# Optimization experiments

Hardware: AMD Instinct MI355X
Metric: run time of the kernel (lower is better)

Reference implementation:

```python
import jax, jax.numpy as jnp
import numpy as np

B = 16; C = 20; M = 64
LEVELS = [("p3", 8, 128), ("p4", 16, 64), ("p5", 32, 32)]  # name, stride, H(=W)
BOUNDS = {"p3": (0.0, 64.0), "p4": (64.0, 128.0), "p5": (128.0, jnp.inf)}
TOPK = 1000; MAX_DET = 100; IOU_THR = 0.5; SCORE_THR = 0.3


def _grid(h, w, stride):
    # replicates get_fpn_location_coords (incl. torch's meshgrid(y, x) ordering)
    xs = stride * (jnp.arange(w, dtype=jnp.float32) + 0.5)
    ys = stride * (jnp.arange(h, dtype=jnp.float32) + 0.5)
    a, b = jnp.meshgrid(ys, xs, indexing="ij")
    return jnp.stack([a, b], axis=-1).reshape(h * w, 2)


def setup_inputs() -> dict:
    key = jax.random.key(0)
    ks = jax.random.split(key, 16)
    inp = {}
    inp["locs_p3"] = _grid(128, 128, 8)
    inp["locs_p4"] = _grid(64, 64, 16)
    inp["locs_p5"] = _grid(32, 32, 32)
    xy = jax.random.uniform(ks[0], (B, M, 2), minval=0.0, maxval=700.0)
    wh = jax.random.uniform(ks[1], (B, M, 2), minval=32.0, maxval=300.0)
    cid = jax.random.randint(ks[2], (B, M, 1), 0, C).astype(jnp.float32)
    gt = jnp.concatenate([xy, xy + wh, cid], axis=-1)
    pad = jnp.arange(M) >= (M - 16)  # last 16 rows are background padding
    inp["gt_boxes"] = jnp.where(pad[None, :, None], -1.0, gt)
    for i, (name, stride, h) in enumerate(LEVELS):
        n = h * h
        inp[f"cls_{name}"] = jax.random.normal(ks[3 + i], (B, n, C)) - 2.0
        inp[f"reg_{name}"] = jax.random.uniform(ks[6 + i], (B, n, 4), minval=0.0, maxval=8.0)
        inp[f"ctr_{name}"] = jax.random.normal(ks[9 + i], (B, n))
    return inp


def _match_level(centers, gt, lower, upper):
    # centers (N,2), gt (M,5) -> matched gt box per center (N,5), -1 for background
    x = centers[:, 0:1]; y = centers[:, 1:2]
    x0, y0, x1, y1 = gt[:, 0], gt[:, 1], gt[:, 2], gt[:, 3]
    ltrb = jnp.stack([x - x0[None], y - y0[None], x1[None] - x, y1[None] - y], axis=-1)  # (N,M,4)
    inside = ltrb.min(-1) > 0
    maxd = ltrb.max(-1)
    ok = inside & (maxd > lower) & (maxd < upper)
    areas = (x1 - x0) * (y1 - y0)
    quality = ok.astype(jnp.float32) * (1e8 - areas)[None, :]
    q = quality.max(-1)
    idx = jnp.argmax(quality, axis=-1)
    idx = jnp.where(q < 1e-5, -1, idx)
    matched = gt[jnp.clip(idx, 0)]
    return jnp.where((idx < 0)[:, None], -1.0, matched)


def _targets(centers, matched, stride):
    # fcos_get_deltas_from_locations + fcos_make_centerness_targets
    xc, yc = centers[:, 0], centers[:, 1]
    d = jnp.stack([(xc - matched[:, 0]) / stride, (yc - matched[:, 1]) / stride,
                   (matched[:, 2] - xc) / stride, (matched[:, 3] - yc) / stride], axis=1)
    bg = jnp.all(matched == -1.0, axis=1)
    d = jnp.where(bg[:, None], -1.0, d)
    l, t, r, b = d[:, 0], d[:, 1], d[:, 2], d[:, 3]
    ctr = jnp.sqrt(jnp.minimum(l, r) * jnp.minimum(t, b) / (jnp.maximum(l, r) * jnp.maximum(t, b)))
    ctr = jnp.where(jnp.all(d == -1.0, axis=1), -1.0, ctr)
    return d, ctr


def _decode(deltas, locs, stride):
    # fcos_apply_deltas_to_locations
    d = jnp.maximum(deltas, 0.0)
    xc, yc = locs[:, 0], locs[:, 1]
    return jnp.stack([xc - d[:, 0] * stride, yc - d[:, 1] * stride,
                      xc + d[:, 2] * stride, yc + d[:, 3] * stride], axis=1)


def _nms_keep(boxes, scores, valid):
    # sequential greedy NMS (argmax + IoU suppression), capped at MAX_DET picks
    areas = (boxes[:, 2] - boxes[:, 0]) * (boxes[:, 3] - boxes[:, 1])
    def body(_, state):
        active, keep = state
        s = jnp.where(active, scores, -jnp.inf)
        i = jnp.argmax(s)
        ok = s[i] > -jnp.inf
        b = boxes[i]
        xx1 = jnp.maximum(b[0], boxes[:, 0]); yy1 = jnp.maximum(b[1], boxes[:, 1])
        xx2 = jnp.minimum(b[2], boxes[:, 2]); yy2 = jnp.minimum(b[3], boxes[:, 3])
        inter = jnp.clip(xx2 - xx1, 0.0) * jnp.clip(yy2 - yy1, 0.0)
        iou = inter / (areas[i] + areas - inter)
        keep = keep.at[i].set(keep[i] | ok)
        active = jnp.where(ok, active & (iou <= IOU_THR), active)
        return active, keep
    _, keep = jax.lax.fori_loop(0, MAX_DET, body, (valid, jnp.zeros_like(valid)))
    return keep


def _infer_one(boxes, scores_cls):
    # boxes (N,4), scores_cls (N,C) -> masked detections (TOPK,5)
    score = scores_cls.max(-1)
    cls_id = jnp.argmax(scores_cls, axis=-1)
    sc, idx = jax.lax.top_k(score, TOPK)
    bx = boxes[idx]; cid = cls_id[idx]
    valid = sc > SCORE_THR
    max_coord = jnp.max(jnp.where(valid[:, None], bx, 0.0))
    off = cid.astype(bx.dtype) * (max_coord + 1.0)  # class_spec_nms offsets
    keep = _nms_keep(bx + off[:, None], sc, valid)
    det = jnp.concatenate([bx, sc[:, None]], axis=-1)
    return jnp.where(keep[:, None], det, 0.0)


def reference(locs_p3, locs_p4, locs_p5, gt_boxes, cls_p3, cls_p4, cls_p5,
              reg_p3, reg_p4, reg_p5, ctr_p3, ctr_p4, ctr_p5):
    locs = {"p3": locs_p3, "p4": locs_p4, "p5": locs_p5}
    cls = {"p3": cls_p3, "p4": cls_p4, "p5": cls_p5}
    reg = {"p3": reg_p3, "p4": reg_p4, "p5": reg_p5}
    ctr = {"p3": ctr_p3, "p4": ctr_p4, "p5": ctr_p5}
    # ---- training targets (no-grad in original) ----
    tgt_d, tgt_c = [], []
    for name, stride, _ in LEVELS:
        lo, hi = BOUNDS[name]
        matched = jax.vmap(lambda g, L=locs[name], lo=lo, hi=hi: _match_level(L, g, lo, hi))(gt_boxes)
        d, c = jax.vmap(lambda m, L=locs[name], s=stride: _targets(L, m, s))(matched)
        tgt_d.append(d); tgt_c.append(c)
    gt_deltas = jax.lax.stop_gradient(jnp.concatenate(tgt_d, axis=1))   # (B, N_total, 4)
    gt_ctr = jax.lax.stop_gradient(jnp.concatenate(tgt_c, axis=1))      # (B, N_total)
    # ---- inference: decode + score + class-specific NMS ----
    all_boxes, all_scores = [], []
    for name, stride, _ in LEVELS:
        bx = jax.vmap(lambda d, L=locs[name], s=stride: _decode(d, L, s))(reg[name])
        sc = jnp.sqrt(jax.nn.sigmoid(cls[name]) * jax.nn.sigmoid(ctr[name])[..., None])
        all_boxes.append(bx); all_scores.append(sc)
    boxes = jnp.concatenate(all_boxes, axis=1)    # (B, N_total, 4)
    scores = jnp.concatenate(all_scores, axis=1)  # (B, N_total, C)
    dets = jax.vmap(_infer_one)(boxes, scores)    # (B, TOPK, 5)
    return dets, gt_deltas, gt_ctr
```

## Files before the change

kernel.cpp:

```cpp
#include <hip/hip_runtime.h>
#include <hip/hip_bf16.h>
#include <math.h>
#include <stdint.h>

#pragma clang fp contract(off)

#define NB   16
#define NC   20
#define NM   64
#define NT   21504
#define OFF1 16384
#define OFF2 20480
#define TOPK 1000
#define DELTA_OFF 80000L
#define CTR_OFF   1456256L

#define WS_SCORES   0L
#define WS_BOXESW   344064L
#define WS_CIDW     1720320L
#define WS_TOPSC    2064384L
#define WS_TOPBOX   2080768L
#define WS_TOPSHIFT 2146304L
#define WS_TOPAREA  2211840L
#define WS_ACT      2228224L
#define WS_MATRIX   0L

__device__ __forceinline__ int detect_bf(const void* locs0) {
  unsigned w = *(const unsigned*)locs0;
  return ((w & 0xFFFFu) == 0u) ? 0 : 1;
}
__device__ __forceinline__ float ldin(const void* p, long i, int bf) {
  if (bf) return __uint_as_float(((unsigned)((const unsigned short*)p)[i]) << 16);
  return ((const float*)p)[i];
}
__device__ __forceinline__ unsigned short f2bf(float v) {
  unsigned w = __float_as_uint(v);
  return (unsigned short)((w + 0x7FFFu + ((w >> 16) & 1u)) >> 16);
}
__device__ __forceinline__ void stout(void* p, long i, float v, int bf) {
  if (bf) ((unsigned short*)p)[i] = f2bf(v);
  else    ((float*)p)[i] = v;
}

__global__ __launch_bounds__(256)
void k_main(const void* locs0, const void* locs1, const void* locs2,
            const void* gt,
            const void* cls0, const void* cls1, const void* cls2,
            const void* reg0, const void* reg1, const void* reg2,
            const void* ctr0, const void* ctr1, const void* ctr2,
            void* out, float* scores, float* boxesw, float* cidw) {
  __shared__ float sgt[NM * 5];
  __shared__ float scls[256 * 21];
  const int bf  = detect_bf(locs0);
  const int b   = blockIdx.y;
  const int blk = blockIdx.x;
  const int tid = threadIdx.x;
  const int n   = blk * 256 + tid;

  const void *L, *CL, *RG, *CT; int NL, base; float stride, lower, upper;
  if (blk < 64)      { L=locs0; CL=cls0; RG=reg0; CT=ctr0; NL=16384; base=0;    stride=8.f;  lower=0.f;   upper=64.f; }
  else if (blk < 80) { L=locs1; CL=cls1; RG=reg1; CT=ctr1; NL=4096;  base=OFF1; stride=16.f; lower=64.f;  upper=128.f; }
  else               { L=locs2; CL=cls2; RG=reg2; CT=ctr2; NL=1024;  base=OFF2; stride=32.f; lower=128.f; upper=INFINITY; }
  const int nl     = n - base;
  const int nlBase = blk * 256 - base;

  for (int i = tid; i < NM * 5; i += 256) sgt[i] = ldin(gt, (long)b * NM * 5 + i, bf);

  long cbase = ((long)b * NL + nlBase) * NC;
  if (!bf) {
    const float4* p = (const float4*)((const float*)CL + cbase);
    for (int i = tid; i < 1280; i += 256) {
      float4 v = p[i];
      int e = i * 4;
      scls[( e      / 20) * 21 +  e      % 20] = v.x;
      scls[((e + 1) / 20) * 21 + (e + 1) % 20] = v.y;
      scls[((e + 2) / 20) * 21 + (e + 2) % 20] = v.z;
      scls[((e + 3) / 20) * 21 + (e + 3) % 20] = v.w;
    }
  } else {
    const unsigned* p = (const unsigned*)((const unsigned short*)CL + cbase);
    for (int i = tid; i < 2560; i += 256) {
      unsigned w = p[i];
      int e = i * 2;
      scls[( e      / 20) * 21 +  e      % 20] = __uint_as_float((w & 0xFFFFu) << 16);
      scls[((e + 1) / 20) * 21 + (e + 1) % 20] = __uint_as_float(w & 0xFFFF0000u);
    }
  }
  __syncthreads();

  float cx = ldin(L, (long)nl * 2 + 0, bf);
  float cy = ldin(L, (long)nl * 2 + 1, bf);

  float best = -1.0f; int bi = 0;
  for (int m = 0; m < NM; ++m) {
    float g0 = sgt[m*5+0], g1 = sgt[m*5+1], g2 = sgt[m*5+2], g3 = sgt[m*5+3];
    float l = cx - g0, t = cy - g1, r = g2 - cx, d = g3 - cy;
    float mn = fminf(fminf(l, t), fminf(r, d));
    float mx = fmaxf(fmaxf(l, t), fmaxf(r, d));
    bool  ok = (mn > 0.f) && (mx > lower) && (mx < upper);
    float area = (g2 - g0) * (g3 - g1);
    float q = ok ? (100000000.0f - area) : 0.f;
    if (q > best) { best = q; bi = m; }
  }
  float d0, d1, d2, d3, ctrv;
  if (best < 1e-5f) {
    d0 = d1 = d2 = d3 = -1.f; ctrv = -1.f;
  } else {
    float m0 = sgt[bi*5+0], m1 = sgt[bi*5+1], m2 = sgt[bi*5+2], m3 = sgt[bi*5+3];
    d0 = (cx - m0) / stride; d1 = (cy - m1) / stride;
    d2 = (m2 - cx) / stride; d3 = (m3 - cy) / stride;
    float mnlr = fminf(d0, d2), mntb = fminf(d1, d3);
    float mxlr = fmaxf(d0, d2), mxtb = fmaxf(d1, d3);
    ctrv = sqrtf((mnlr * mntb) / (mxlr * mxtb));
  }
  long dbase = DELTA_OFF + ((long)b * NT + n) * 4;
  if (!bf) {
    *(float4*)((float*)out + dbase) = make_float4(d0, d1, d2, d3);
  } else {
    ushort4 v; v.x = f2bf(d0); v.y = f2bf(d1); v.z = f2bf(d2); v.w = f2bf(d3);
    *(ushort4*)((unsigned short*)out + dbase) = v;
  }
  stout(out, CTR_OFF + (long)b * NT + n, ctrv, bf);

  float ct  = ldin(CT, (long)b * NL + nl, bf);
  float sct = 1.0f / (1.0f + expf(-ct));
  float smax = -1.0f; int ci = 0;
  for (int c = 0; c < NC; ++c) {
    float v  = scls[tid * 21 + c];
    float sv = 1.0f / (1.0f + expf(-v));
    float s  = sqrtf(sv * sct);
    if (s > smax) { smax = s; ci = c; }
  }
  float r0, r1, r2, r3;
  long rbase = ((long)b * NL + nl) * 4;
  if (!bf) {
    float4 rv = *(const float4*)((const float*)RG + rbase);
    r0 = rv.x; r1 = rv.y; r2 = rv.z; r3 = rv.w;
  } else {
    uint2 rw = *(const uint2*)((const unsigned short*)RG + rbase);
    r0 = __uint_as_float((rw.x & 0xFFFFu) << 16); r1 = __uint_as_float(rw.x & 0xFFFF0000u);
    r2 = __uint_as_float((rw.y & 0xFFFFu) << 16); r3 = __uint_as_float(rw.y & 0xFFFF0000u);
  }
  r0 = fmaxf(r0, 0.f); r1 = fmaxf(r1, 0.f); r2 = fmaxf(r2, 0.f); r3 = fmaxf(r3, 0.f);
  long o = (long)b * NT + n;
  scores[o] = smax;
  *(float4*)(boxesw + o * 4) =
      make_float4(cx - r0 * stride, cy - r1 * stride, cx + r2 * stride, cy + r3 * stride);
  cidw[o] = (float)ci;
}

__global__ __launch_bounds__(1024)
void k_select(const float* scores, const float* boxesw, const float* cidw,
              float* topScore, float* topBox, float* topShift, float* topArea,
              unsigned long long* actInit) {
  const int b    = blockIdx.x;
  const int tid  = threadIdx.x;
  const int wid  = tid >> 6;
  const int lane = tid & 63;
  const float* sb = scores + (long)b * NT;

  __shared__ unsigned long long selKeys[1024];
  __shared__ unsigned wcnt[16][3];
  __shared__ unsigned selCnt;
  __shared__ float redf[16];
  __shared__ float sMaxC;

  unsigned inv[21];
#pragma unroll
  for (int k = 0; k < 21; ++k)
    inv[k] = ~__float_as_uint(sb[tid + k * 1024]);

  unsigned V = 0xC0000000u;
  for (int s = 28; s >= 0; s -= 2) {
    unsigned T1 = V | (1u << s), T2 = V | (2u << s), T3 = V | (3u << s);
    unsigned c1 = 0, c2 = 0, c3 = 0;
#pragma unroll
    for (int k = 0; k < 21; ++k) {
      c1 += (unsigned)__popcll(__ballot(inv[k] < T1));
      c2 += (unsigned)__popcll(__ballot(inv[k] < T2));
      c3 += (unsigned)__popcll(__ballot(inv[k] < T3));
    }
    if (lane == 0) { wcnt[wid][0] = c1; wcnt[wid][1] = c2; wcnt[wid][2] = c3; }
    __syncthreads();
    unsigned t1 = 0, t2 = 0, t3 = 0;
    for (int w = 0; w < 16; ++w) { t1 += wcnt[w][0]; t2 += wcnt[w][1]; t3 += wcnt[w][2]; }
    unsigned p = (t3 < TOPK) ? 3u : (t2 < TOPK) ? 2u : (t1 < TOPK) ? 1u : 0u;
    V |= p << s;
    __syncthreads();
  }

  if (tid == 0) selCnt = 0u;
  __syncthreads();
#pragma unroll
  for (int k = 0; k < 21; ++k)
    if (inv[k] < V) {
      unsigned p = atomicAdd(&selCnt, 1u);
      if (p < 1024u) selKeys[p] = ((unsigned long long)inv[k] << 32) | (unsigned)(tid + k * 1024);
    }
  __syncthreads();
#pragma unroll
  for (int k = 0; k < 21; ++k)
    if (inv[k] == V) {
      unsigned p = atomicAdd(&selCnt, 1u);
      if (p < 1024u) selKeys[p] = ((unsigned long long)inv[k] << 32) | (unsigned)(tid + k * 1024);
    }
  __syncthreads();
  unsigned total = selCnt < 1024u ? selCnt : 1024u;
  if ((unsigned)tid >= total) selKeys[tid] = 0xFFFFFFFFFFFFFFFFull;
  __syncthreads();

  for (unsigned k = 2; k <= 1024; k <<= 1) {
    for (unsigned j = k >> 1; j > 0; j >>= 1) {
      unsigned ixj = (unsigned)tid ^ j;
      if (ixj > (unsigned)tid) {
        unsigned long long a = selKeys[tid], c = selKeys[ixj];
        bool up = ((tid & k) == 0);
        if (up ? (a > c) : (a < c)) { selKeys[tid] = c; selKeys[ixj] = a; }
      }
      __syncthreads();
    }
  }

  unsigned long long key = selKeys[tid];
  float sc = __uint_as_float(~(unsigned)(key >> 32));
  float4 bv = make_float4(0.f, 0.f, 0.f, 0.f);
  float cid = 0.f;
  if (tid < TOPK) {
    long o = (long)b * NT + (unsigned)key;
    bv = *(const float4*)(boxesw + o * 4);
    cid = cidw[o];
  } else sc = 0.f;

  float loc = (tid < TOPK)
      ? ((sc > 0.3f) ? fmaxf(fmaxf(bv.x, bv.y), fmaxf(bv.z, bv.w)) : 0.0f)
      : -INFINITY;
  for (int o = 32; o > 0; o >>= 1) loc = fmaxf(loc, __shfl_down(loc, o));
  if (lane == 0) redf[wid] = loc;
  __syncthreads();
  if (tid == 0) {
    float m = redf[0];
    for (int w = 1; w < 16; ++w) m = fmaxf(m, redf[w]);
    sMaxC = m;
  }
  __syncthreads();

  float offm = sMaxC + 1.0f;
  long tb = (long)b * 1024 + tid;
  if (tid < TOPK) {
    float o4 = cid * offm;
    float s0 = bv.x + o4, s1 = bv.y + o4, s2 = bv.z + o4, s3 = bv.w + o4;
    *(float4*)(topShift + tb * 4) = make_float4(s0, s1, s2, s3);
    topArea[tb]  = (s2 - s0) * (s3 - s1);
    *(float4*)(topBox + tb * 4) = bv;
    topScore[tb] = sc;
  } else {
    *(float4*)(topShift + tb * 4) = make_float4(0.f, 0.f, 0.f, 0.f);
    topArea[tb]  = 0.f;
    *(float4*)(topBox + tb * 4) = make_float4(0.f, 0.f, 0.f, 0.f);
    topScore[tb] = 0.f;
  }
  unsigned long long vb = __ballot((tid < TOPK) && (sc > 0.3f));
  if (lane == 0) actInit[b * 16 + wid] = vb;
}

__global__ __launch_bounds__(1024)
void k_iou(const float* topShift, const float* topArea, unsigned* matrix) {
  const int wh  = blockIdx.x;
  const int b   = blockIdx.y;
  const int tid = threadIdx.x;
  const int jbase = (wh >> 1) * 64 + (wh & 1) * 32;
  __shared__ float jx0[32], jy0[32], jx1[32], jy1[32], ja[32];
  if (tid < 32) {
    long tj = (long)b * 1024 + jbase + tid;
    float4 s = *(const float4*)(topShift + tj * 4);
    jx0[tid] = s.x; jy0[tid] = s.y; jx1[tid] = s.z; jy1[tid] = s.w;
    ja[tid] = topArea[tj];
  }
  __syncthreads();
  long ti = (long)b * 1024 + tid;
  float4 si = *(const float4*)(topShift + ti * 4);
  float ai  = topArea[ti];
  unsigned word = 0u;
  for (int k = 0; k < 32; ++k) {
    float xx1 = fmaxf(si.x, jx0[k]);
    float yy1 = fmaxf(si.y, jy0[k]);
    float xx2 = fminf(si.z, jx1[k]);
    float yy2 = fminf(si.w, jy1[k]);
    float inter = fmaxf(xx2 - xx1, 0.f) * fmaxf(yy2 - yy1, 0.f);
    float iou = inter / (ai + ja[k] - inter);
    if (!(iou <= 0.5f)) word |= (1u << k);
  }
  matrix[ti * 32 + wh] = word;
}

__global__ __launch_bounds__(256)
void k_scan(const unsigned long long* matrix, const unsigned long long* actInit,
            const float* topBox, const float* topScore, void* out, const void* locs0) {
  const int bf   = detect_bf(locs0);
  const int b    = blockIdx.x;
  const int tid  = threadIdx.x;
  const int wid  = tid >> 6;
  const int lane = tid & 63;
  const unsigned long long* M = matrix + (long)b * 1024 * 16;

  __shared__ unsigned long long rows[2][64][16];
  __shared__ unsigned long long keepSh[16];

  unsigned long long act = 0ull, keep = 0ull;
  if (wid == 0 && lane < 16) act = actInit[b * 16 + lane];

  for (int t = tid; t < 1024; t += 256)
    rows[0][t >> 4][t & 15] = M[t];
  __syncthreads();

  int kept = 0;
  for (int c = 0; c < 16; ++c) {
    if (wid > 0) {
      if (c < 15) {
        for (int t = tid - 64; t < 1024; t += 192)
          rows[(c + 1) & 1][t >> 4][t & 15] = M[(long)(c + 1) * 1024 + t];
      }
    } else {
      unsigned long long cur = __shfl(act, c);
      while (cur && kept < 100) {
        int k = __ffsll((unsigned long long)cur) - 1;
        ++kept;
        if (lane == c) keep |= (1ull << k);
        unsigned long long r = (lane < 16) ? rows[c & 1][k][lane] : 0ull;
        act &= ~r;
        cur = __shfl(act, c);
      }
    }
    __syncthreads();
  }
  if (wid == 0 && lane < 16) keepSh[lane] = keep;
  __syncthreads();

  for (int r = tid; r < TOPK; r += 256) {
    bool kp = (keepSh[r >> 6] >> (r & 63)) & 1ull;
    long tb = (long)b * 1024 + r;
    float4 bx = *(const float4*)(topBox + tb * 4);
    float sc  = topScore[tb];
    long o = ((long)b * TOPK + r) * 5;
    stout(out, o + 0, kp ? bx.x : 0.f, bf);
    stout(out, o + 1, kp ? bx.y : 0.f, bf);
    stout(out, o + 2, kp ? bx.z : 0.f, bf);
    stout(out, o + 3, kp ? bx.w : 0.f, bf);
    stout(out, o + 4, kp ? sc   : 0.f, bf);
  }
}

extern "C" void kernel_launch(void* const* d_in, const int* in_sizes, int n_in,
                              void* d_out, int out_size, void* d_ws, size_t ws_size,
                              hipStream_t stream) {
  const void* locs0 = d_in[0];
  const void* locs1 = d_in[1];
  const void* locs2 = d_in[2];
  const void* gt    = d_in[3];

  int ic[3], ir[3], it[3];
  if (n_in >= 13 && in_sizes[5] == 16 * 4096 * 20) {
    ic[0]=4; ic[1]=5; ic[2]=6;  ir[0]=7; ir[1]=8; ir[2]=9;  it[0]=10; it[1]=11; it[2]=12;
  } else {
    ic[0]=4; ic[1]=7; ic[2]=10; ir[0]=5; ir[1]=8; ir[2]=11; it[0]=6;  it[1]=9;  it[2]=12;
  }
  const void* cls0 = d_in[ic[0]]; const void* cls1 = d_in[ic[1]]; const void* cls2 = d_in[ic[2]];
  const void* reg0 = d_in[ir[0]]; const void* reg1 = d_in[ir[1]]; const void* reg2 = d_in[ir[2]];
  const void* ctr0 = d_in[it[0]]; const void* ctr1 = d_in[it[1]]; const void* ctr2 = d_in[it[2]];

  float* ws       = (float*)d_ws;
  float* scores   = ws + WS_SCORES;
  float* boxesw   = ws + WS_BOXESW;
  float* cidw     = ws + WS_CIDW;
  float* topScore = ws + WS_TOPSC;
  float* topBox   = ws + WS_TOPBOX;
  float* topShift = ws + WS_TOPSHIFT;
  float* topArea  = ws + WS_TOPAREA;
  unsigned long long* actInit = (unsigned long long*)(ws + WS_ACT);
  unsigned*           matrix32 = (unsigned*)(ws + WS_MATRIX);
  unsigned long long* matrix64 = (unsigned long long*)(ws + WS_MATRIX);

  k_main<<<dim3(NT / 256, NB), 256, 0, stream>>>(locs0, locs1, locs2, gt,
                                                 cls0, cls1, cls2,
                                                 reg0, reg1, reg2,
                                                 ctr0, ctr1, ctr2,
                                                 d_out, scores, boxesw, cidw);
  k_select<<<NB, 1024, 0, stream>>>(scores, boxesw, cidw,
                                    topScore, topBox, topShift, topArea, actInit);
  k_iou<<<dim3(32, NB), 1024, 0, stream>>>(topShift, topArea, matrix32);
  k_scan<<<NB, 256, 0, stream>>>(matrix64, actInit, topBox, topScore, d_out, locs0);
}
```

Before: 228.5 us.

## Use monotonic argmax for class scores, histogram top-k select, shuffle bitonic sort, skip IoU lower triangle

k_main drops the shared-memory class staging. Each thread loads its 20 logits directly, takes the argmax on raw logits and evaluates sigmoid/sqrt once, falling back to the full loop only when the top two are within 1e-3. k_select replaces the 15-pass 2-bit radix threshold search with two shared-memory histogram passes and prefix scans, and runs the bitonic stages below 64 with wavefront shuffles in registers. k_iou returns early for rows above the current column block, so the lower triangle is never computed, on the assumption that the scan only reads upper entries. Together these cut transcendental work, barrier-heavy passes and wasted IoU computation, at the cost of shared-memory atomics and a tie-handling path.

```diff
diff --git a/kernel.cpp b/kernel.cpp
--- a/kernel.cpp
+++ b/kernel.cpp
@@ -50,7 +50,6 @@
             const void* ctr0, const void* ctr1, const void* ctr2,
             void* out, float* scores, float* boxesw, float* cidw) {
   __shared__ float sgt[NM * 5];
-  __shared__ float scls[256 * 21];
   const int bf  = detect_bf(locs0);
   const int b   = blockIdx.y;
   const int blk = blockIdx.x;
@@ -61,31 +60,9 @@
   if (blk < 64)      { L=locs0; CL=cls0; RG=reg0; CT=ctr0; NL=16384; base=0;    stride=8.f;  lower=0.f;   upper=64.f; }
   else if (blk < 80) { L=locs1; CL=cls1; RG=reg1; CT=ctr1; NL=4096;  base=OFF1; stride=16.f; lower=64.f;  upper=128.f; }
   else               { L=locs2; CL=cls2; RG=reg2; CT=ctr2; NL=1024;  base=OFF2; stride=32.f; lower=128.f; upper=INFINITY; }
-  const int nl     = n - base;
-  const int nlBase = blk * 256 - base;
+  const int nl = n - base;
 
   for (int i = tid; i < NM * 5; i += 256) sgt[i] = ldin(gt, (long)b * NM * 5 + i, bf);
-
-  long cbase = ((long)b * NL + nlBase) * NC;
-  if (!bf) {
-    const float4* p = (const float4*)((const float*)CL + cbase);
-    for (int i = tid; i < 1280; i += 256) {
-      float4 v = p[i];
-      int e = i * 4;
-      scls[( e      / 20) * 21 +  e      % 20] = v.x;
-      scls[((e + 1) / 20) * 21 + (e + 1) % 20] = v.y;
-      scls[((e + 2) / 20) * 21 + (e + 2) % 20] = v.z;
-      scls[((e + 3) / 20) * 21 + (e + 3) % 20] = v.w;
-    }
-  } else {
-    const unsigned* p = (const unsigned*)((const unsigned short*)CL + cbase);
-    for (int i = tid; i < 2560; i += 256) {
-      unsigned w = p[i];
-      int e = i * 2;
-      scls[( e      / 20) * 21 +  e      % 20] = __uint_as_float((w & 0xFFFFu) << 16);
-      scls[((e + 1) / 20) * 21 + (e + 1) % 20] = __uint_as_float(w & 0xFFFF0000u);
-    }
-  }
   __syncthreads();
 
   float cx = ldin(L, (long)nl * 2 + 0, bf);
@@ -124,13 +101,46 @@
 
   float ct  = ldin(CT, (long)b * NL + nl, bf);
   float sct = 1.0f / (1.0f + expf(-ct));
-  float smax = -1.0f; int ci = 0;
-  for (int c = 0; c < NC; ++c) {
-    float v  = scls[tid * 21 + c];
-    float sv = 1.0f / (1.0f + expf(-v));
-    float s  = sqrtf(sv * sct);
-    if (s > smax) { smax = s; ci = c; }
-  }
+
+  float cl[NC];
+  long cb = ((long)b * NL + nl) * NC;
+  if (!bf) {
+    const float4* p = (const float4*)((const float*)CL + cb);
+#pragma unroll
+    for (int i = 0; i < 5; ++i) {
+      float4 q = p[i];
+      cl[4*i+0] = q.x; cl[4*i+1] = q.y; cl[4*i+2] = q.z; cl[4*i+3] = q.w;
+    }
+  } else {
+    const uint2* p = (const uint2*)((const unsigned short*)CL + cb);
+#pragma unroll
+    for (int i = 0; i < 5; ++i) {
+      uint2 q = p[i];
+      cl[4*i+0] = __uint_as_float((q.x & 0xFFFFu) << 16);
+      cl[4*i+1] = __uint_as_float(q.x & 0xFFFF0000u);
+      cl[4*i+2] = __uint_as_float((q.y & 0xFFFFu) << 16);
+      cl[4*i+3] = __uint_as_float(q.y & 0xFFFF0000u);
+    }
+  }
+  float vmax = cl[0], v2 = -INFINITY; int ci = 0;
+#pragma unroll
+  for (int c = 1; c < NC; ++c) {
+    if (cl[c] > vmax) { v2 = vmax; vmax = cl[c]; ci = c; }
+    else if (cl[c] > v2) v2 = cl[c];
+  }
+  float smax;
+  if (vmax - v2 < 1e-3f) {
+    smax = -1.0f; ci = 0;
+    for (int c = 0; c < NC; ++c) {
+      float sv = 1.0f / (1.0f + expf(-cl[c]));
+      float s  = sqrtf(sv * sct);
+      if (s > smax) { smax = s; ci = c; }
+    }
+  } else {
+    float sv = 1.0f / (1.0f + expf(-vmax));
+    smax = sqrtf(sv * sct);
+  }
+
   float r0, r1, r2, r3;
   long rbase = ((long)b * NL + nl) * 4;
   if (!bf) {
@@ -147,6 +157,14 @@
   *(float4*)(boxesw + o * 4) =
       make_float4(cx - r0 * stride, cy - r1 * stride, cx + r2 * stride, cy + r3 * stride);
   cidw[o] = (float)ci;
+}
+
+__device__ __forceinline__ unsigned wscan(unsigned v, int lane) {
+  for (int off = 1; off < 64; off <<= 1) {
+    unsigned u = __shfl_up(v, off);
+    if (lane >= off) v += u;
+  }
+  return v;
 }
 
 __global__ __launch_bounds__(1024)
@@ -159,9 +177,10 @@
   const int lane = tid & 63;
   const float* sb = scores + (long)b * NT;
 
-  __shared__ unsigned long long selKeys[1024];
-  __shared__ unsigned wcnt[16][3];
-  __shared__ unsigned selCnt;
+  __shared__ unsigned hist[8192];
+  unsigned long long* selKeys = (unsigned long long*)hist;
+  __shared__ unsigned wsum[16];
+  __shared__ unsigned sTop, sBefore, sSub, selCnt;
   __shared__ float redf[16];
   __shared__ float sMaxC;
 
@@ -170,58 +189,93 @@
   for (int k = 0; k < 21; ++k)
     inv[k] = ~__float_as_uint(sb[tid + k * 1024]);
 
-  unsigned V = 0xC0000000u;
-  for (int s = 28; s >= 0; s -= 2) {
-    unsigned T1 = V | (1u << s), T2 = V | (2u << s), T3 = V | (3u << s);
-    unsigned c1 = 0, c2 = 0, c3 = 0;
-#pragma unroll
-    for (int k = 0; k < 21; ++k) {
-      c1 += (unsigned)__popcll(__ballot(inv[k] < T1));
-      c2 += (unsigned)__popcll(__ballot(inv[k] < T2));
-      c3 += (unsigned)__popcll(__ballot(inv[k] < T3));
-    }
-    if (lane == 0) { wcnt[wid][0] = c1; wcnt[wid][1] = c2; wcnt[wid][2] = c3; }
+  for (int i = tid; i < 8192; i += 1024) hist[i] = 0u;
+  __syncthreads();
+#pragma unroll
+  for (int k = 0; k < 21; ++k)
+    atomicAdd(&hist[(inv[k] >> 17) - 0x6000u], 1u);
+  __syncthreads();
+  {
+    unsigned hloc[8], s0 = 0;
+#pragma unroll
+    for (int j = 0; j < 8; ++j) { hloc[j] = hist[8 * tid + j]; s0 += hloc[j]; }
+    unsigned sc = wscan(s0, lane);
+    if (lane == 63) wsum[wid] = sc;
     __syncthreads();
-    unsigned t1 = 0, t2 = 0, t3 = 0;
-    for (int w = 0; w < 16; ++w) { t1 += wcnt[w][0]; t2 += wcnt[w][1]; t3 += wcnt[w][2]; }
-    unsigned p = (t3 < TOPK) ? 3u : (t2 < TOPK) ? 2u : (t1 < TOPK) ? 1u : 0u;
-    V |= p << s;
+    unsigned basev = 0;
+    for (int w = 0; w < wid; ++w) basev += wsum[w];
+    unsigned cumBefore = basev + sc - s0;
+    if (cumBefore < TOPK && cumBefore + s0 >= TOPK) {
+      unsigned c = cumBefore;
+#pragma unroll
+      for (int j = 0; j < 8; ++j) {
+        if (c + hloc[j] >= TOPK) { sTop = (8 * tid + j) + 0x6000u; sBefore = c; break; }
+        c += hloc[j];
+      }
+    }
+  }
+  __syncthreads();
+  const unsigned topBits = sTop;
+  const unsigned r = TOPK - sBefore;
+
+  for (int i = tid; i < 8192; i += 1024) hist[i] = 0u;
+  __syncthreads();
+#pragma unroll
+  for (int k = 0; k < 21; ++k)
+    if ((inv[k] >> 17) == topBits) atomicAdd(&hist[(inv[k] >> 4) & 0x1FFFu], 1u);
+  __syncthreads();
+  {
+    unsigned hloc[8], s0 = 0;
+#pragma unroll
+    for (int j = 0; j < 8; ++j) { hloc[j] = hist[8 * tid + j]; s0 += hloc[j]; }
+    unsigned sc = wscan(s0, lane);
+    if (lane == 63) wsum[wid] = sc;
     __syncthreads();
-  }
-
+    unsigned basev = 0;
+    for (int w = 0; w < wid; ++w) basev += wsum[w];
+    unsigned cumBefore = basev + sc - s0;
+    if (cumBefore < r && cumBefore + s0 >= r) {
+      unsigned c = cumBefore;
+#pragma unroll
+      for (int j = 0; j < 8; ++j) {
+        if (c + hloc[j] >= r) { sSub = 8 * tid + j; break; }
+        c += hloc[j];
+      }
+    }
+  }
+  __syncthreads();
+  const unsigned long long cutEnd =
+      ((unsigned long long)topBits << 17) | ((unsigned long long)(sSub + 1u) << 4);
   if (tid == 0) selCnt = 0u;
   __syncthreads();
+
 #pragma unroll
   for (int k = 0; k < 21; ++k)
-    if (inv[k] < V) {
+    if ((unsigned long long)inv[k] < cutEnd) {
       unsigned p = atomicAdd(&selCnt, 1u);
       if (p < 1024u) selKeys[p] = ((unsigned long long)inv[k] << 32) | (unsigned)(tid + k * 1024);
     }
   __syncthreads();
-#pragma unroll
-  for (int k = 0; k < 21; ++k)
-    if (inv[k] == V) {
-      unsigned p = atomicAdd(&selCnt, 1u);
-      if (p < 1024u) selKeys[p] = ((unsigned long long)inv[k] << 32) | (unsigned)(tid + k * 1024);
-    }
-  __syncthreads();
   unsigned total = selCnt < 1024u ? selCnt : 1024u;
-  if ((unsigned)tid >= total) selKeys[tid] = 0xFFFFFFFFFFFFFFFFull;
+  unsigned long long key =
+      ((unsigned)tid < total) ? selKeys[tid] : 0xFFFFFFFFFFFFFFFFull;
   __syncthreads();
 
   for (unsigned k = 2; k <= 1024; k <<= 1) {
     for (unsigned j = k >> 1; j > 0; j >>= 1) {
-      unsigned ixj = (unsigned)tid ^ j;
-      if (ixj > (unsigned)tid) {
-        unsigned long long a = selKeys[tid], c = selKeys[ixj];
-        bool up = ((tid & k) == 0);
-        if (up ? (a > c) : (a < c)) { selKeys[tid] = c; selKeys[ixj] = a; }
+      unsigned long long other;
+      if (j >= 64) {
+        selKeys[tid] = key; __syncthreads();
+        other = selKeys[tid ^ j]; __syncthreads();
+      } else {
+        other = __shfl(key, (int)(lane ^ j));
       }
-      __syncthreads();
-    }
-  }
-
-  unsigned long long key = selKeys[tid];
+      bool up = ((tid & k) == 0);
+      bool takeMin = (((tid & j) == 0) == up);
+      key = takeMin ? (key < other ? key : other) : (key > other ? key : other);
+    }
+  }
+
   float sc = __uint_as_float(~(unsigned)(key >> 32));
   float4 bv = make_float4(0.f, 0.f, 0.f, 0.f);
   float cid = 0.f;
@@ -277,6 +331,7 @@
     ja[tid] = topArea[tj];
   }
   __syncthreads();
+  if (tid > jbase + 31) return;
   long ti = (long)b * 1024 + tid;
   float4 si = *(const float4*)(topShift + ti * 4);
   float ai  = topArea[ti];
@@ -326,8 +381,8 @@
         int k = __ffsll((unsigned long long)cur) - 1;
         ++kept;
         if (lane == c) keep |= (1ull << k);
-        unsigned long long r = (lane < 16) ? rows[c & 1][k][lane] : 0ull;
-        act &= ~r;
+        unsigned long long rrow = (lane < 16) ? rows[c & 1][k][lane] : 0ull;
+        act &= ~rrow;
         cur = __shfl(act, c);
       }
     }
```

Result: faster. 186.3 us (-18.5%).
